# Optimization experiments

Hardware: AMD Instinct MI355X
Metric: run time of the kernel (lower is better)

## Reference

```python
import jax, jax.numpy as jnp
import numpy as np

L = 2          # num_hidden_layers
B, S, H = 2, 2048, 1024
NH, DH = 16, 64   # heads, head dim
FF = 4096
EPS = 1e-5


def setup_inputs() -> dict:
    key = jax.random.key(0)
    ks = jax.random.split(key, 20)
    s = 0.02
    inp = {
        "hidden_states": jax.random.normal(ks[0], (B, S, H), jnp.float32),
        "attention_mask": jnp.zeros((B, 1, 1, S), jnp.float32),
        "Wq": jax.random.normal(ks[1], (L, H, H), jnp.float32) * s,
        "bq": jnp.zeros((L, H), jnp.float32),
        "Wk": jax.random.normal(ks[2], (L, H, H), jnp.float32) * s,
        "bk": jnp.zeros((L, H), jnp.float32),
        "Wv": jax.random.normal(ks[3], (L, H, H), jnp.float32) * s,
        "bv": jnp.zeros((L, H), jnp.float32),
        "Wao": jax.random.normal(ks[4], (L, H, H), jnp.float32) * s,
        "bao": jnp.zeros((L, H), jnp.float32),
        "ln1_g": jnp.ones((L, H), jnp.float32),
        "ln1_b": jnp.zeros((L, H), jnp.float32),
        "Wi": jax.random.normal(ks[5], (L, H, FF), jnp.float32) * s,
        "bi": jnp.zeros((L, FF), jnp.float32),
        "Wo": jax.random.normal(ks[6], (L, FF, H), jnp.float32) * s,
        "bo": jnp.zeros((L, H), jnp.float32),
        "ln2_g": jnp.ones((L, H), jnp.float32),
        "ln2_b": jnp.zeros((L, H), jnp.float32),
    }
    return inp


def _layernorm(x, g, b):
    m = jnp.mean(x, axis=-1, keepdims=True)
    v = jnp.var(x, axis=-1, keepdims=True)
    return (x - m) * jax.lax.rsqrt(v + EPS) * g + b


def _split_heads(x):
    # [B,S,H] -> [B,NH,S,DH]
    return x.reshape(B, S, NH, DH).transpose(0, 2, 1, 3)


def _layer(x, mask, Wq, bq, Wk, bk, Wv, bv, Wao, bao, g1, b1, Wi, bi, Wo, bo, g2, b2):
    q = _split_heads(x @ Wq + bq)
    k = _split_heads(x @ Wk + bk)
    v = _split_heads(x @ Wv + bv)
    scores = jnp.einsum('bhqd,bhkd->bhqk', q, k) / np.sqrt(DH).astype(np.float32)
    scores = scores + mask  # additive attention mask
    probs = jax.nn.softmax(scores, axis=-1)
    ctx = jnp.einsum('bhqk,bhkd->bhqd', probs, v)
    ctx = ctx.transpose(0, 2, 1, 3).reshape(B, S, H)
    x = _layernorm(ctx @ Wao + bao + x, g1, b1)
    ffn = jax.nn.gelu(x @ Wi + bi, approximate=False) @ Wo + bo
    return _layernorm(ffn + x, g2, b2)


def reference(hidden_states, attention_mask, Wq, bq, Wk, bk, Wv, bv, Wao, bao,
              ln1_g, ln1_b, Wi, bi, Wo, bo, ln2_g, ln2_b):
    x = hidden_states
    for i in range(L):
        x = _layer(x, attention_mask,
                   Wq[i], bq[i], Wk[i], bk[i], Wv[i], bv[i], Wao[i], bao[i],
                   ln1_g[i], ln1_b[i], Wi[i], bi[i], Wo[i], bo[i], ln2_g[i], ln2_b[i])
    return x
```

## Files before the change

### kernel.cpp

```cpp
#include <hip/hip_runtime.h>

typedef _Float16 half_t;
typedef _Float16 half8  __attribute__((ext_vector_type(8)));
typedef _Float16 half4v __attribute__((ext_vector_type(4)));
typedef float    f32x4  __attribute__((ext_vector_type(4)));

#define AS1 __attribute__((address_space(1)))
#define AS3 __attribute__((address_space(3)))

#define MODE_H16  0
#define MODE_F32R 1
#define MODE_GELU 2

__device__ __forceinline__ f32x4 zero4() {
    f32x4 z; z[0] = 0.f; z[1] = 0.f; z[2] = 0.f; z[3] = 0.f; return z;
}

__device__ __forceinline__ half8 lds_frag(const half_t* p) {
    union { uint4 u; half8 h; } c;
    c.u = *(const uint4*)p;
    return c.h;
}

__device__ __forceinline__ float gelu_f(float v) {
    float t = v * v;
    float u = v * (1.595769122f + 0.0713548163f * t);
    return v / (1.f + __expf(-u));
}

__device__ __forceinline__ void gl_lds16(const half_t* g, half_t* l) {
    __builtin_amdgcn_global_load_lds(
        (AS1 unsigned int*)(unsigned long long)(const void*)g,
        (AS3 unsigned int*)l,
        16, 0, 0);
}


__global__ __launch_bounds__(256) void gemm_bt(
    const half_t* __restrict__ A,
    const half_t* __restrict__ Bt,
    const float*  __restrict__ bias,
    const float*  __restrict__ res,
    void* __restrict__ out,
    int M, int N, int K, int mode)
{
    __shared__ __align__(16) half_t As[128 * 64];
    __shared__ __align__(16) half_t Bs[128 * 64];

    const int tid  = threadIdx.x;
    const int w    = tid >> 6, lane = tid & 63;
    const int m0   = blockIdx.y * 128, n0 = blockIdx.x * 128;
    const int g    = lane >> 4, ml = lane & 15, m7 = ml & 7;
    const int mo   = (w >> 1) * 64, no = (w & 1) * 64;
    const int r8   = lane >> 3;
    const int sck  = ((lane & 7) ^ (r8 & 7)) * 8;

    f32x4 acc[4][4];
#pragma unroll
    for (int i = 0; i < 4; i++)
#pragma unroll
        for (int j = 0; j < 4; j++) acc[i][j] = zero4();

    const half_t* Ag = A  + (size_t)m0 * K;
    const half_t* Bg = Bt + (size_t)n0 * K;

    for (int k0 = 0; k0 < K; k0 += 64) {
        __syncthreads();
#pragma unroll
        for (int i = 0; i < 4; i++) {
            int t = w * 4 + i;
            gl_lds16(Ag + (size_t)(t * 8 + r8) * K + k0 + sck, &As[t * 512]);
            gl_lds16(Bg + (size_t)(t * 8 + r8) * K + k0 + sck, &Bs[t * 512]);
        }
        __syncthreads();
#pragma unroll
        for (int kk = 0; kk < 2; kk++) {
            const int co = ((kk * 4 + g) ^ m7) * 8;
            half8 af[4], bf[4];
#pragma unroll
            for (int i = 0; i < 4; i++) af[i] = lds_frag(&As[(mo + i * 16 + ml) * 64 + co]);
#pragma unroll
            for (int j = 0; j < 4; j++) bf[j] = lds_frag(&Bs[(no + j * 16 + ml) * 64 + co]);
#pragma unroll
            for (int i = 0; i < 4; i++)
#pragma unroll
                for (int j = 0; j < 4; j++)
                    acc[i][j] = __builtin_amdgcn_mfma_f32_16x16x32_f16(af[i], bf[j], acc[i][j], 0, 0, 0);
        }
    }

    const int gm0 = m0 + mo, gn0 = n0 + no;
#pragma unroll
    for (int j = 0; j < 4; j++) {
        int col = gn0 + j * 16 + ml;
        float bv = bias[col];
#pragma unroll
        for (int i = 0; i < 4; i++) {
#pragma unroll
            for (int r = 0; r < 4; r++) {
                int row = gm0 + i * 16 + g * 4 + r;
                float v = acc[i][j][r] + bv;
                size_t idx = (size_t)row * N + col;
                if (mode == MODE_F32R) {
                    ((float*)out)[idx] = v + res[idx];
                } else if (mode == MODE_GELU) {
                    ((half_t*)out)[idx] = (half_t)gelu_f(v);
                } else {
                    ((half_t*)out)[idx] = (half_t)v;
                }
            }
        }
    }
}

__global__ __launch_bounds__(256) void gemm_bt64(
    const half_t* __restrict__ A,
    const half_t* __restrict__ Bt,
    const float*  __restrict__ bias,
    const float*  __restrict__ res,
    float* __restrict__ out,
    int M, int N, int K)
{
    __shared__ __align__(16) half_t As[128 * 64];
    __shared__ __align__(16) half_t Bs[64 * 64];

    const int tid  = threadIdx.x;
    const int w    = tid >> 6, lane = tid & 63;
    const int m0   = blockIdx.y * 128, n0 = blockIdx.x * 64;
    const int g    = lane >> 4, ml = lane & 15, m7 = ml & 7;
    const int mo   = w * 32;
    const int r8   = lane >> 3;
    const int sck  = ((lane & 7) ^ (r8 & 7)) * 8;

    f32x4 acc[2][4];
#pragma unroll
    for (int i = 0; i < 2; i++)
#pragma unroll
        for (int j = 0; j < 4; j++) acc[i][j] = zero4();

    const half_t* Ag = A  + (size_t)m0 * K;
    const half_t* Bg = Bt + (size_t)n0 * K;

    for (int k0 = 0; k0 < K; k0 += 64) {
        __syncthreads();
#pragma unroll
        for (int i = 0; i < 4; i++) {
            int t = w * 4 + i;
            gl_lds16(Ag + (size_t)(t * 8 + r8) * K + k0 + sck, &As[t * 512]);
        }
#pragma unroll
        for (int i = 0; i < 2; i++) {
            int t = w * 2 + i;
            gl_lds16(Bg + (size_t)(t * 8 + r8) * K + k0 + sck, &Bs[t * 512]);
        }
        __syncthreads();
#pragma unroll
        for (int kk = 0; kk < 2; kk++) {
            const int co = ((kk * 4 + g) ^ m7) * 8;
            half8 af[2], bf[4];
#pragma unroll
            for (int i = 0; i < 2; i++) af[i] = lds_frag(&As[(mo + i * 16 + ml) * 64 + co]);
#pragma unroll
            for (int j = 0; j < 4; j++) bf[j] = lds_frag(&Bs[(j * 16 + ml) * 64 + co]);
#pragma unroll
            for (int i = 0; i < 2; i++)
#pragma unroll
                for (int j = 0; j < 4; j++)
                    acc[i][j] = __builtin_amdgcn_mfma_f32_16x16x32_f16(af[i], bf[j], acc[i][j], 0, 0, 0);
        }
    }

    const int gm0 = m0 + mo;
#pragma unroll
    for (int j = 0; j < 4; j++) {
        int col = n0 + j * 16 + ml;
        float bv = bias[col];
#pragma unroll
        for (int i = 0; i < 2; i++) {
#pragma unroll
            for (int r = 0; r < 4; r++) {
                int row = gm0 + i * 16 + g * 4 + r;
                size_t idx = (size_t)row * N + col;
                out[idx] = acc[i][j][r] + bv + res[idx];
            }
        }
    }
}

__global__ __launch_bounds__(256) void gemm_qkv(
    const half_t* __restrict__ A,
    const half_t* __restrict__ Bt,
    const float*  __restrict__ bq,
    const float*  __restrict__ bk,
    const float*  __restrict__ bv,
    half_t* __restrict__ Qo, half_t* __restrict__ Ko, half_t* __restrict__ Vto,
    int M, int K)
{
    __shared__ __align__(16) half_t As[128 * 64];
    __shared__ __align__(16) half_t Bs[128 * 64];

    const int tid  = threadIdx.x;
    const int w    = tid >> 6, lane = tid & 63;
    const int m0   = blockIdx.y * 128, n0 = blockIdx.x * 128;
    const int g    = lane >> 4, ml = lane & 15, m7 = ml & 7;
    const int mo   = (w >> 1) * 64, no = (w & 1) * 64;
    const int r8   = lane >> 3;
    const int sck  = ((lane & 7) ^ (r8 & 7)) * 8;

    f32x4 acc[4][4];
#pragma unroll
    for (int i = 0; i < 4; i++)
#pragma unroll
        for (int j = 0; j < 4; j++) acc[i][j] = zero4();

    const half_t* Ag = A  + (size_t)m0 * K;
    const half_t* Bg = Bt + (size_t)n0 * K;

    for (int k0 = 0; k0 < K; k0 += 64) {
        __syncthreads();
#pragma unroll
        for (int i = 0; i < 4; i++) {
            int t = w * 4 + i;
            gl_lds16(Ag + (size_t)(t * 8 + r8) * K + k0 + sck, &As[t * 512]);
            gl_lds16(Bg + (size_t)(t * 8 + r8) * K + k0 + sck, &Bs[t * 512]);
        }
        __syncthreads();
#pragma unroll
        for (int kk = 0; kk < 2; kk++) {
            const int co = ((kk * 4 + g) ^ m7) * 8;
            half8 af[4], bf[4];
#pragma unroll
            for (int i = 0; i < 4; i++) af[i] = lds_frag(&As[(mo + i * 16 + ml) * 64 + co]);
#pragma unroll
            for (int j = 0; j < 4; j++) bf[j] = lds_frag(&Bs[(no + j * 16 + ml) * 64 + co]);
#pragma unroll
            for (int i = 0; i < 4; i++)
#pragma unroll
                for (int j = 0; j < 4; j++)
                    acc[i][j] = __builtin_amdgcn_mfma_f32_16x16x32_f16(af[i], bf[j], acc[i][j], 0, 0, 0);
        }
    }

    const int seg  = n0 >> 10;
    const int nloc = (n0 & 1023) + no;
    const float* bias = (seg == 0) ? bq : (seg == 1) ? bk : bv;
    const int gm0 = m0 + mo;

    if (seg < 2) {
        half_t* O = (seg == 0) ? Qo : Ko;
#pragma unroll
        for (int j = 0; j < 4; j++) {
            int col = nloc + j * 16 + ml;
            float bvv = bias[col];
#pragma unroll
            for (int i = 0; i < 4; i++)
#pragma unroll
                for (int r = 0; r < 4; r++)
                    O[(size_t)(gm0 + i * 16 + g * 4 + r) * 1024 + col] =
                        (half_t)(acc[i][j][r] + bvv);
        }
    } else {
#pragma unroll
        for (int j = 0; j < 4; j++) {
            int col = nloc + j * 16 + ml;
            float bvv = bias[col];
#pragma unroll
            for (int i = 0; i < 4; i++) {
                int rowb = gm0 + i * 16 + g * 4;
                int bb = rowb >> 11, sl = rowb & 2047;
                half4v v;
#pragma unroll
                for (int r = 0; r < 4; r++) v[r] = (half_t)(acc[i][j][r] + bvv);
                *(half4v*)&Vto[((size_t)bb * 1024 + col) * 2048 + sl] = v;
            }
        }
    }
}

__global__ __launch_bounds__(256, 4) void flash_attn(
    const half_t* __restrict__ Q,
    const half_t* __restrict__ Kq,
    const half_t* __restrict__ Vt,
    const float*  __restrict__ mask,
    half_t* __restrict__ opart,
    float2* __restrict__ mlpart,
    int S, int H)
{
    __shared__ __align__(16) half_t Ks[64 * 64];
    __shared__ __align__(16) half_t Vs[64 * 64];
    __shared__ __align__(16) half_t Ps[4 * 32 * 64];

    const int qt = blockIdx.x, h = blockIdx.y, z = blockIdx.z;
    const int b = z >> 1, hf = z & 1;
    const int tid = threadIdx.x, w = tid >> 6, lane = tid & 63;
    const int g = lane >> 4, ml = lane & 15, m7 = ml & 7;
    const int NHloc = gridDim.y;
    const int BNHS = 2 * NHloc * S;

    const int q0 = qt * 128 + w * 32;
    const half_t* Qg = Q  + ((size_t)(b * S + q0)) * H + h * 64;
    const half_t* Kg = Kq + ((size_t)b * S) * H + h * 64;
    const half_t* Vg = Vt + ((size_t)b * H + h * 64) * (size_t)S;
    const float*  mk = mask + (size_t)b * S;

    half8 qf[2][2];
#pragma unroll
    for (int qi = 0; qi < 2; qi++)
#pragma unroll
        for (int kk = 0; kk < 2; kk++)
            qf[qi][kk] = *(const half8*)(Qg + (size_t)(qi * 16 + ml) * H + kk * 32 + g * 8);

    float m_[2] = {-1e30f, -1e30f}, l_[2] = {0.f, 0.f};
    f32x4 o[2][4];
#pragma unroll
    for (int qi = 0; qi < 2; qi++)
#pragma unroll
        for (int df = 0; df < 4; df++) o[qi][df] = zero4();

    half_t* Pw = &Ps[w * 32 * 64];
    const int srow = tid >> 3;
    const int sc   = tid & 7;

    const int kvbeg = hf * (S >> 1), kvend = kvbeg + (S >> 1);
    for (int kv0 = kvbeg; kv0 < kvend; kv0 += 64) {
        __syncthreads();
#pragma unroll
        for (int t = 0; t < 2; t++) {
            int row = t * 32 + srow;
            int ck  = sc ^ (row & 7);
            gl_lds16(Kg + (size_t)(kv0 + row) * H + ck * 8, &Ks[(t * 256 + w * 64) * 8]);
            gl_lds16(Vg + (size_t)row * S + kv0 + ck * 8,   &Vs[(t * 256 + w * 64) * 8]);
        }
        __syncthreads();

        f32x4 s[2][4];
#pragma unroll
        for (int kvf = 0; kvf < 4; kvf++) {
            half8 k0 = lds_frag(&Ks[(kvf * 16 + ml) * 64 + ((0 + g) ^ m7) * 8]);
            half8 k1 = lds_frag(&Ks[(kvf * 16 + ml) * 64 + ((4 + g) ^ m7) * 8]);
            s[0][kvf] = __builtin_amdgcn_mfma_f32_16x16x32_f16(k0, qf[0][0], zero4(), 0, 0, 0);
            s[0][kvf] = __builtin_amdgcn_mfma_f32_16x16x32_f16(k1, qf[0][1], s[0][kvf], 0, 0, 0);
            s[1][kvf] = __builtin_amdgcn_mfma_f32_16x16x32_f16(k0, qf[1][0], zero4(), 0, 0, 0);
            s[1][kvf] = __builtin_amdgcn_mfma_f32_16x16x32_f16(k1, qf[1][1], s[1][kvf], 0, 0, 0);
        }
#pragma unroll
        for (int kvf = 0; kvf < 4; kvf++) {
            float4 mv = *(const float4*)(mk + kv0 + kvf * 16 + g * 4);
#pragma unroll
            for (int qi = 0; qi < 2; qi++) {
                s[qi][kvf][0] = s[qi][kvf][0] * 0.125f + mv.x;
                s[qi][kvf][1] = s[qi][kvf][1] * 0.125f + mv.y;
                s[qi][kvf][2] = s[qi][kvf][2] * 0.125f + mv.z;
                s[qi][kvf][3] = s[qi][kvf][3] * 0.125f + mv.w;
            }
        }
        float alpha[2];
#pragma unroll
        for (int qi = 0; qi < 2; qi++) {
            float mx = -1e30f;
#pragma unroll
            for (int kvf = 0; kvf < 4; kvf++)
#pragma unroll
                for (int r = 0; r < 4; r++) mx = fmaxf(mx, s[qi][kvf][r]);
            mx = fmaxf(mx, __shfl_xor(mx, 16));
            mx = fmaxf(mx, __shfl_xor(mx, 32));
            float mnew = fmaxf(m_[qi], mx);
            alpha[qi]  = __expf(m_[qi] - mnew);
            m_[qi] = mnew;
            float ps = 0.f;
#pragma unroll
            for (int kvf = 0; kvf < 4; kvf++)
#pragma unroll
                for (int r = 0; r < 4; r++) {
                    float pv = __expf(s[qi][kvf][r] - mnew);
                    s[qi][kvf][r] = pv; ps += pv;
                }
            ps += __shfl_xor(ps, 16);
            ps += __shfl_xor(ps, 32);
            l_[qi] = l_[qi] * alpha[qi] + ps;
#pragma unroll
            for (int kvf = 0; kvf < 4; kvf++) {
                half4v pk;
#pragma unroll
                for (int r = 0; r < 4; r++) pk[r] = (half_t)s[qi][kvf][r];
                *(half4v*)(Pw + (qi * 16 + ml) * 64 +
                           (((kvf * 2 + (g >> 1)) ^ m7) * 8) + (g & 1) * 4) = pk;
            }
        }
#pragma unroll
        for (int qi = 0; qi < 2; qi++) {
#pragma unroll
            for (int r = 0; r < 4; r++) {
                float a = __shfl(alpha[qi], (lane & 48) + g * 4 + r);
#pragma unroll
                for (int df = 0; df < 4; df++) o[qi][df][r] *= a;
            }
        }
#pragma unroll
        for (int kk = 0; kk < 2; kk++) {
            half8 pa0 = lds_frag(&Pw[(ml)      * 64 + ((kk * 4 + g) ^ m7) * 8]);
            half8 pa1 = lds_frag(&Pw[(16 + ml) * 64 + ((kk * 4 + g) ^ m7) * 8]);
#pragma unroll
            for (int df = 0; df < 4; df++) {
                half8 vb = lds_frag(&Vs[(df * 16 + ml) * 64 + ((kk * 4 + g) ^ m7) * 8]);
                o[0][df] = __builtin_amdgcn_mfma_f32_16x16x32_f16(pa0, vb, o[0][df], 0, 0, 0);
                o[1][df] = __builtin_amdgcn_mfma_f32_16x16x32_f16(pa1, vb, o[1][df], 0, 0, 0);
            }
        }
    }

    const size_t rowbase = (size_t)hf * BNHS + ((size_t)(b * NHloc + h)) * S + q0;
#pragma unroll
    for (int qi = 0; qi < 2; qi++) {
#pragma unroll
        for (int r = 0; r < 4; r++) {
            size_t ro = (rowbase + qi * 16 + g * 4 + r) * 64;
#pragma unroll
            for (int df = 0; df < 4; df++)
                opart[ro + df * 16 + ml] = (half_t)o[qi][df][r];
        }
    }
    if (g == 0) {
#pragma unroll
        for (int qi = 0; qi < 2; qi++)
            mlpart[rowbase + qi * 16 + ml] = make_float2(m_[qi], l_[qi]);
    }
}

__global__ __launch_bounds__(256) void flash_merge(
    const half_t* __restrict__ opart,
    const float2* __restrict__ mlpart,
    half_t* __restrict__ ctx)
{
    int gid = blockIdx.x * 256 + threadIdx.x;
    int row = gid >> 4, dg = (gid & 15) * 4;
    float2 a = mlpart[row], c = mlpart[65536 + row];
    float m  = fmaxf(a.x, c.x);
    float w1 = __expf(a.x - m), w2 = __expf(c.x - m);
    float inv = 1.f / (w1 * a.y + w2 * c.y);
    half4v o1 = *(const half4v*)&opart[(size_t)row * 64 + dg];
    half4v o2 = *(const half4v*)&opart[(size_t)(65536 + row) * 64 + dg];
    int b = row >> 15, hq = row & 32767;
    int h = hq >> 11, q = hq & 2047;
    half4v o;
#pragma unroll
    for (int i = 0; i < 4; i++)
        o[i] = (half_t)((w1 * (float)o1[i] + w2 * (float)o2[i]) * inv);
    *(half4v*)&ctx[((size_t)(b * 2048 + q)) * 1024 + h * 64 + dg] = o;
}

__global__ __launch_bounds__(256) void transpose_cast(
    const float* __restrict__ W, half_t* __restrict__ Wt, int Kd, int Nd)
{
    __shared__ float tile[32][33];
    size_t zoff = (size_t)blockIdx.z * Kd * Nd;
    const float* Wz = W + zoff;
    half_t* Wtz = Wt + zoff;
    int n0 = blockIdx.x * 32, k0 = blockIdx.y * 32;
    int tx = threadIdx.x & 31, ty = threadIdx.x >> 5;
#pragma unroll
    for (int j = 0; j < 4; j++)
        tile[ty + j * 8][tx] = Wz[(size_t)(k0 + ty + j * 8) * Nd + n0 + tx];
    __syncthreads();
#pragma unroll
    for (int j = 0; j < 4; j++)
        Wtz[(size_t)(n0 + ty + j * 8) * Kd + k0 + tx] = (half_t)tile[tx][ty + j * 8];
}

__global__ __launch_bounds__(256) void transpose_qkv(
    const float* __restrict__ Wq, const float* __restrict__ Wk,
    const float* __restrict__ Wv, half_t* __restrict__ WT)
{
    __shared__ float tile[32][33];
    int z = blockIdx.z, l = z / 3, which = z % 3;
    const float* W = ((which == 0) ? Wq : (which == 1) ? Wk : Wv) + (size_t)l * 1024 * 1024;
    half_t* D = WT + ((size_t)l * 3 + which) * 1024 * 1024;
    int n0 = blockIdx.x * 32, k0 = blockIdx.y * 32;
    int tx = threadIdx.x & 31, ty = threadIdx.x >> 5;
#pragma unroll
    for (int j = 0; j < 4; j++)
        tile[ty + j * 8][tx] = W[(size_t)(k0 + ty + j * 8) * 1024 + n0 + tx];
    __syncthreads();
#pragma unroll
    for (int j = 0; j < 4; j++)
        D[(size_t)(n0 + ty + j * 8) * 1024 + k0 + tx] = (half_t)tile[tx][ty + j * 8];
}

__global__ __launch_bounds__(256) void cast_f32_f16(
    const float* __restrict__ in, half_t* __restrict__ out)
{
    int i = blockIdx.x * 256 + threadIdx.x;
    float4 v = ((const float4*)in)[i];
    half4v o; o[0] = (half_t)v.x; o[1] = (half_t)v.y; o[2] = (half_t)v.z; o[3] = (half_t)v.w;
    *(half4v*)(out + (size_t)i * 4) = o;
}

__global__ __launch_bounds__(256) void layernorm_k(
    const float* __restrict__ in,
    const float* __restrict__ gam, const float* __restrict__ bet,
    float* __restrict__ outf, half_t* __restrict__ outh)
{
    int row = blockIdx.x, tid = threadIdx.x;
    const float4 v = ((const float4*)(in + (size_t)row * 1024))[tid];
    float s = v.x + v.y + v.z + v.w;
    float q = v.x * v.x + v.y * v.y + v.z * v.z + v.w * v.w;
    for (int off = 32; off; off >>= 1) { s += __shfl_down(s, off); q += __shfl_down(q, off); }
    __shared__ float ss[4], sq[4];
    int w = tid >> 6;
    if ((tid & 63) == 0) { ss[w] = s; sq[w] = q; }
    __syncthreads();
    float S_ = ss[0] + ss[1] + ss[2] + ss[3];
    float Q_ = sq[0] + sq[1] + sq[2] + sq[3];
    float mean = S_ * (1.f / 1024.f);
    float var  = Q_ * (1.f / 1024.f) - mean * mean;
    float rstd = rsqrtf(var + 1e-5f);
    float4 gm = ((const float4*)gam)[tid];
    float4 bt = ((const float4*)bet)[tid];
    float y0 = (v.x - mean) * rstd * gm.x + bt.x;
    float y1 = (v.y - mean) * rstd * gm.y + bt.y;
    float y2 = (v.z - mean) * rstd * gm.z + bt.z;
    float y3 = (v.w - mean) * rstd * gm.w + bt.w;
    ((float4*)(outf + (size_t)row * 1024))[tid] = make_float4(y0, y1, y2, y3);
    half4v oh; oh[0] = (half_t)y0; oh[1] = (half_t)y1; oh[2] = (half_t)y2; oh[3] = (half_t)y3;
    *(half4v*)(outh + (size_t)row * 1024 + tid * 4) = oh;
}

extern "C" void kernel_launch(void* const* d_in, const int* in_sizes, int n_in,
                              void* d_out, int out_size, void* d_ws, size_t ws_size,
                              hipStream_t stream)
{
    const int Lc = 2, Bb = 2, S = 2048, Hh = 1024, NH = 16, FF = 4096;
    const int M = Bb * S;

    const float* hs   = (const float*)d_in[0];
    const float* mask = (const float*)d_in[1];
    const float* Wq   = (const float*)d_in[2];  const float* bq  = (const float*)d_in[3];
    const float* Wk   = (const float*)d_in[4];  const float* bk  = (const float*)d_in[5];
    const float* Wv   = (const float*)d_in[6];  const float* bv  = (const float*)d_in[7];
    const float* Wao  = (const float*)d_in[8];  const float* bao = (const float*)d_in[9];
    const float* g1   = (const float*)d_in[10]; const float* b1  = (const float*)d_in[11];
    const float* Wi   = (const float*)d_in[12]; const float* bi  = (const float*)d_in[13];
    const float* Wo   = (const float*)d_in[14]; const float* bo  = (const float*)d_in[15];
    const float* g2   = (const float*)d_in[16]; const float* b2  = (const float*)d_in[17];

    char* p = (char*)d_ws;
    auto take = [&](size_t bytes) { char* r = p; p += (bytes + 255) & ~(size_t)255; return r; };

    half_t* WqkvT = (half_t*)take((size_t)Lc * 3 * Hh * Hh * 2);
    half_t* WaoT  = (half_t*)take((size_t)Lc * Hh * Hh * 2);
    half_t* WiT   = (half_t*)take((size_t)Lc * Hh * FF * 2);
    half_t* WoT   = (half_t*)take((size_t)Lc * FF * Hh * 2);
    half_t* xb    = (half_t*)take((size_t)M * Hh * 2);
    half_t* Qb    = (half_t*)take((size_t)M * Hh * 2);
    half_t* Kb2   = (half_t*)take((size_t)M * Hh * 2);
    half_t* Vtb   = (half_t*)take((size_t)M * Hh * 2);
    (void)          take((size_t)M * Hh * 2);
    half_t* h1    = Qb;
    float*  t0    = (float*)take((size_t)M * Hh * 4);
    float*  x1f   = (float*)take((size_t)M * Hh * 4);
    half_t* x1b   = (half_t*)take((size_t)M * Hh * 2);

    half_t* opart  = (half_t*)t0;
    float2* mlpart = (float2*)x1b;

    dim3 tb(256);

    transpose_qkv<<<dim3(32, 32, Lc * 3), tb, 0, stream>>>(Wq, Wk, Wv, WqkvT);
    transpose_cast<<<dim3(32, 32, Lc), tb, 0, stream>>>(Wao, WaoT, Hh, Hh);
    transpose_cast<<<dim3(FF / 32, 32, Lc), tb, 0, stream>>>(Wi, WiT, Hh, FF);
    transpose_cast<<<dim3(32, FF / 32, Lc), tb, 0, stream>>>(Wo, WoT, FF, Hh);
    cast_f32_f16<<<dim3(M * Hh / 1024), tb, 0, stream>>>(hs, xb);

    const float* xres = hs;
    for (int l = 0; l < Lc; l++) {
        const half_t* WqkvTl = WqkvT + (size_t)l * 3 * Hh * Hh;
        const half_t* WaoTl  = WaoT  + (size_t)l * Hh * Hh;
        const half_t* WiTl   = WiT   + (size_t)l * Hh * FF;
        const half_t* WoTl   = WoT   + (size_t)l * FF * Hh;

        gemm_qkv<<<dim3(3072 / 128, M / 128), tb, 0, stream>>>(
            xb, WqkvTl, bq + l * Hh, bk + l * Hh, bv + l * Hh, Qb, Kb2, Vtb, M, Hh);

        flash_attn<<<dim3(S / 128, NH, Bb * 2), tb, 0, stream>>>(
            Qb, Kb2, Vtb, mask, opart, mlpart, S, Hh);
        flash_merge<<<dim3(Bb * NH * S * 16 / 256), tb, 0, stream>>>(opart, mlpart, xb);

        gemm_bt64<<<dim3(Hh / 64, M / 128), tb, 0, stream>>>(
            xb, WaoTl, bao + l * Hh, xres, t0, M, Hh, Hh);
        layernorm_k<<<dim3(M), tb, 0, stream>>>(t0, g1 + l * Hh, b1 + l * Hh, x1f, x1b);

        gemm_bt<<<dim3(FF / 128, M / 128), tb, 0, stream>>>(
            x1b, WiTl, bi + l * FF, nullptr, h1, M, FF, Hh, MODE_GELU);
        gemm_bt64<<<dim3(Hh / 64, M / 128), tb, 0, stream>>>(
            h1, WoTl, bo + l * Hh, x1f, t0, M, Hh, FF);

        float* outf = (l == Lc - 1) ? (float*)d_out : x1f;
        layernorm_k<<<dim3(M), tb, 0, stream>>>(t0, g2 + l * Hh, b2 + l * Hh, outf, xb);
        xres = x1f;
    }
}
```

Measured before the change: 717.5 us.

## Double-buffer GEMM LDS tiles with K=32 stages and new swizzle

All three GEMM kernels now split each 64-wide K step into two 32-wide LDS stages held in a ping-pong buffer. The next stage's global-to-LDS load is issued before computing on the current one, so memory latency overlaps with MFMA work. The swizzle changes to fit 32-element rows, and launch bounds now request 4 blocks per CU to keep occupancy. The cost is a barrier per 32-wide half-step instead of two per 64-wide step, plus a different LDS bank-conflict pattern.

```diff
diff --git a/kernel.cpp b/kernel.cpp
--- a/kernel.cpp
+++ b/kernel.cpp
@@ -36,7 +36,7 @@
 }
 
 
-__global__ __launch_bounds__(256) void gemm_bt(
+__global__ __launch_bounds__(256, 4) void gemm_bt(
     const half_t* __restrict__ A,
     const half_t* __restrict__ Bt,
     const float*  __restrict__ bias,
@@ -44,16 +44,17 @@
     void* __restrict__ out,
     int M, int N, int K, int mode)
 {
-    __shared__ __align__(16) half_t As[128 * 64];
-    __shared__ __align__(16) half_t Bs[128 * 64];
+    __shared__ __align__(16) half_t As[2][128 * 32];
+    __shared__ __align__(16) half_t Bs[2][128 * 32];
 
     const int tid  = threadIdx.x;
     const int w    = tid >> 6, lane = tid & 63;
     const int m0   = blockIdx.y * 128, n0 = blockIdx.x * 128;
-    const int g    = lane >> 4, ml = lane & 15, m7 = ml & 7;
+    const int g    = lane >> 4, ml = lane & 15;
     const int mo   = (w >> 1) * 64, no = (w & 1) * 64;
-    const int r8   = lane >> 3;
-    const int sck  = ((lane & 7) ^ (r8 & 7)) * 8;
+    const int lr   = lane >> 2;
+    const int sck  = (((lane & 3) ^ (lr & 3) ^ ((lr >> 2) & 3)) * 8);
+    const int co   = ((g ^ (ml & 3) ^ ((ml >> 2) & 3)) * 8);
 
     f32x4 acc[4][4];
 #pragma unroll
@@ -64,29 +65,36 @@
     const half_t* Ag = A  + (size_t)m0 * K;
     const half_t* Bg = Bt + (size_t)n0 * K;
 
+    auto stage = [&](int p, int k0) {
+#pragma unroll
+        for (int i = 0; i < 2; i++) {
+            int t = w * 2 + i;
+            gl_lds16(Ag + (size_t)(t * 16 + lr) * K + k0 + sck, &As[p][t * 512]);
+            gl_lds16(Bg + (size_t)(t * 16 + lr) * K + k0 + sck, &Bs[p][t * 512]);
+        }
+    };
+    auto compute = [&](int p) {
+        half8 af[4], bf[4];
+#pragma unroll
+        for (int i = 0; i < 4; i++) af[i] = lds_frag(&As[p][(mo + i * 16 + ml) * 32 + co]);
+#pragma unroll
+        for (int j = 0; j < 4; j++) bf[j] = lds_frag(&Bs[p][(no + j * 16 + ml) * 32 + co]);
+#pragma unroll
+        for (int i = 0; i < 4; i++)
+#pragma unroll
+            for (int j = 0; j < 4; j++)
+                acc[i][j] = __builtin_amdgcn_mfma_f32_16x16x32_f16(af[i], bf[j], acc[i][j], 0, 0, 0);
+    };
+
+    stage(0, 0);
+    __syncthreads();
     for (int k0 = 0; k0 < K; k0 += 64) {
-        __syncthreads();
-#pragma unroll
-        for (int i = 0; i < 4; i++) {
-            int t = w * 4 + i;
-            gl_lds16(Ag + (size_t)(t * 8 + r8) * K + k0 + sck, &As[t * 512]);
-            gl_lds16(Bg + (size_t)(t * 8 + r8) * K + k0 + sck, &Bs[t * 512]);
-        }
-        __syncthreads();
-#pragma unroll
-        for (int kk = 0; kk < 2; kk++) {
-            const int co = ((kk * 4 + g) ^ m7) * 8;
-            half8 af[4], bf[4];
-#pragma unroll
-            for (int i = 0; i < 4; i++) af[i] = lds_frag(&As[(mo + i * 16 + ml) * 64 + co]);
-#pragma unroll
-            for (int j = 0; j < 4; j++) bf[j] = lds_frag(&Bs[(no + j * 16 + ml) * 64 + co]);
-#pragma unroll
-            for (int i = 0; i < 4; i++)
-#pragma unroll
-                for (int j = 0; j < 4; j++)
-                    acc[i][j] = __builtin_amdgcn_mfma_f32_16x16x32_f16(af[i], bf[j], acc[i][j], 0, 0, 0);
-        }
+        stage(1, k0 + 32);
+        compute(0);
+        __syncthreads();
+        if (k0 + 64 < K) stage(0, k0 + 64);
+        compute(1);
+        __syncthreads();
     }
 
     const int gm0 = m0 + mo, gn0 = n0 + no;
@@ -113,7 +121,7 @@
     }
 }
 
-__global__ __launch_bounds__(256) void gemm_bt64(
+__global__ __launch_bounds__(256, 4) void gemm_bt64(
     const half_t* __restrict__ A,
     const half_t* __restrict__ Bt,
     const float*  __restrict__ bias,
@@ -121,16 +129,17 @@
     float* __restrict__ out,
     int M, int N, int K)
 {
-    __shared__ __align__(16) half_t As[128 * 64];
-    __shared__ __align__(16) half_t Bs[64 * 64];
+    __shared__ __align__(16) half_t As[2][128 * 32];
+    __shared__ __align__(16) half_t Bs[2][64 * 32];
 
     const int tid  = threadIdx.x;
     const int w    = tid >> 6, lane = tid & 63;
     const int m0   = blockIdx.y * 128, n0 = blockIdx.x * 64;
-    const int g    = lane >> 4, ml = lane & 15, m7 = ml & 7;
+    const int g    = lane >> 4, ml = lane & 15;
     const int mo   = w * 32;
-    const int r8   = lane >> 3;
-    const int sck  = ((lane & 7) ^ (r8 & 7)) * 8;
+    const int lr   = lane >> 2;
+    const int sck  = (((lane & 3) ^ (lr & 3) ^ ((lr >> 2) & 3)) * 8);
+    const int co   = ((g ^ (ml & 3) ^ ((ml >> 2) & 3)) * 8);
 
     f32x4 acc[2][4];
 #pragma unroll
@@ -141,33 +150,36 @@
     const half_t* Ag = A  + (size_t)m0 * K;
     const half_t* Bg = Bt + (size_t)n0 * K;
 
-    for (int k0 = 0; k0 < K; k0 += 64) {
-        __syncthreads();
-#pragma unroll
-        for (int i = 0; i < 4; i++) {
-            int t = w * 4 + i;
-            gl_lds16(Ag + (size_t)(t * 8 + r8) * K + k0 + sck, &As[t * 512]);
-        }
+    auto stage = [&](int p, int k0) {
 #pragma unroll
         for (int i = 0; i < 2; i++) {
             int t = w * 2 + i;
-            gl_lds16(Bg + (size_t)(t * 8 + r8) * K + k0 + sck, &Bs[t * 512]);
-        }
-        __syncthreads();
-#pragma unroll
-        for (int kk = 0; kk < 2; kk++) {
-            const int co = ((kk * 4 + g) ^ m7) * 8;
-            half8 af[2], bf[4];
-#pragma unroll
-            for (int i = 0; i < 2; i++) af[i] = lds_frag(&As[(mo + i * 16 + ml) * 64 + co]);
-#pragma unroll
-            for (int j = 0; j < 4; j++) bf[j] = lds_frag(&Bs[(j * 16 + ml) * 64 + co]);
-#pragma unroll
-            for (int i = 0; i < 2; i++)
-#pragma unroll
-                for (int j = 0; j < 4; j++)
-                    acc[i][j] = __builtin_amdgcn_mfma_f32_16x16x32_f16(af[i], bf[j], acc[i][j], 0, 0, 0);
-        }
+            gl_lds16(Ag + (size_t)(t * 16 + lr) * K + k0 + sck, &As[p][t * 512]);
+        }
+        gl_lds16(Bg + (size_t)(w * 16 + lr) * K + k0 + sck, &Bs[p][w * 512]);
+    };
+    auto compute = [&](int p) {
+        half8 af[2], bf[4];
+#pragma unroll
+        for (int i = 0; i < 2; i++) af[i] = lds_frag(&As[p][(mo + i * 16 + ml) * 32 + co]);
+#pragma unroll
+        for (int j = 0; j < 4; j++) bf[j] = lds_frag(&Bs[p][(j * 16 + ml) * 32 + co]);
+#pragma unroll
+        for (int i = 0; i < 2; i++)
+#pragma unroll
+            for (int j = 0; j < 4; j++)
+                acc[i][j] = __builtin_amdgcn_mfma_f32_16x16x32_f16(af[i], bf[j], acc[i][j], 0, 0, 0);
+    };
+
+    stage(0, 0);
+    __syncthreads();
+    for (int k0 = 0; k0 < K; k0 += 64) {
+        stage(1, k0 + 32);
+        compute(0);
+        __syncthreads();
+        if (k0 + 64 < K) stage(0, k0 + 64);
+        compute(1);
+        __syncthreads();
     }
 
     const int gm0 = m0 + mo;
@@ -187,7 +199,7 @@
     }
 }
 
-__global__ __launch_bounds__(256) void gemm_qkv(
+__global__ __launch_bounds__(256, 4) void gemm_qkv(
     const half_t* __restrict__ A,
     const half_t* __restrict__ Bt,
     const float*  __restrict__ bq,
@@ -196,16 +208,17 @@
     half_t* __restrict__ Qo, half_t* __restrict__ Ko, half_t* __restrict__ Vto,
     int M, int K)
 {
-    __shared__ __align__(16) half_t As[128 * 64];
-    __shared__ __align__(16) half_t Bs[128 * 64];
+    __shared__ __align__(16) half_t As[2][128 * 32];
+    __shared__ __align__(16) half_t Bs[2][128 * 32];
 
     const int tid  = threadIdx.x;
     const int w    = tid >> 6, lane = tid & 63;
     const int m0   = blockIdx.y * 128, n0 = blockIdx.x * 128;
-    const int g    = lane >> 4, ml = lane & 15, m7 = ml & 7;
+    const int g    = lane >> 4, ml = lane & 15;
     const int mo   = (w >> 1) * 64, no = (w & 1) * 64;
-    const int r8   = lane >> 3;
-    const int sck  = ((lane & 7) ^ (r8 & 7)) * 8;
+    const int lr   = lane >> 2;
+    const int sck  = (((lane & 3) ^ (lr & 3) ^ ((lr >> 2) & 3)) * 8);
+    const int co   = ((g ^ (ml & 3) ^ ((ml >> 2) & 3)) * 8);
 
     f32x4 acc[4][4];
 #pragma unroll
@@ -216,29 +229,36 @@
     const half_t* Ag = A  + (size_t)m0 * K;
     const half_t* Bg = Bt + (size_t)n0 * K;
 
+    auto stage = [&](int p, int k0) {
+#pragma unroll
+        for (int i = 0; i < 2; i++) {
+            int t = w * 2 + i;
+            gl_lds16(Ag + (size_t)(t * 16 + lr) * K + k0 + sck, &As[p][t * 512]);
+            gl_lds16(Bg + (size_t)(t * 16 + lr) * K + k0 + sck, &Bs[p][t * 512]);
+        }
+    };
+    auto compute = [&](int p) {
+        half8 af[4], bf[4];
+#pragma unroll
+        for (int i = 0; i < 4; i++) af[i] = lds_frag(&As[p][(mo + i * 16 + ml) * 32 + co]);
+#pragma unroll
+        for (int j = 0; j < 4; j++) bf[j] = lds_frag(&Bs[p][(no + j * 16 + ml) * 32 + co]);
+#pragma unroll
+        for (int i = 0; i < 4; i++)
+#pragma unroll
+            for (int j = 0; j < 4; j++)
+                acc[i][j] = __builtin_amdgcn_mfma_f32_16x16x32_f16(af[i], bf[j], acc[i][j], 0, 0, 0);
+    };
+
+    stage(0, 0);
+    __syncthreads();
     for (int k0 = 0; k0 < K; k0 += 64) {
-        __syncthreads();
-#pragma unroll
-        for (int i = 0; i < 4; i++) {
-            int t = w * 4 + i;
-            gl_lds16(Ag + (size_t)(t * 8 + r8) * K + k0 + sck, &As[t * 512]);
-            gl_lds16(Bg + (size_t)(t * 8 + r8) * K + k0 + sck, &Bs[t * 512]);
-        }
-        __syncthreads();
-#pragma unroll
-        for (int kk = 0; kk < 2; kk++) {
-            const int co = ((kk * 4 + g) ^ m7) * 8;
-            half8 af[4], bf[4];
-#pragma unroll
-            for (int i = 0; i < 4; i++) af[i] = lds_frag(&As[(mo + i * 16 + ml) * 64 + co]);
-#pragma unroll
-            for (int j = 0; j < 4; j++) bf[j] = lds_frag(&Bs[(no + j * 16 + ml) * 64 + co]);
-#pragma unroll
-            for (int i = 0; i < 4; i++)
-#pragma unroll
-                for (int j = 0; j < 4; j++)
-                    acc[i][j] = __builtin_amdgcn_mfma_f32_16x16x32_f16(af[i], bf[j], acc[i][j], 0, 0, 0);
-        }
+        stage(1, k0 + 32);
+        compute(0);
+        __syncthreads();
+        if (k0 + 64 < K) stage(0, k0 + 64);
+        compute(1);
+        __syncthreads();
     }
 
     const int seg  = n0 >> 10;
```

New measurement: 772.1 us. +7.6%, slower.
